# Performance work log

Hardware: AMD Instinct MI355X
Metric: run time of the kernel (lower is better)

Reference implementation:

```python
import jax, jax.numpy as jnp
import numpy as np
from jax import lax

N, C, H, W = 6, 64, 128, 128
BN_EPS = 1e-5


def setup_inputs() -> dict:
    key = jax.random.key(0)
    ks = jax.random.split(key, 16)
    def p(i, shape, scale=0.05):
        return jax.random.normal(ks[i], shape, jnp.float32) * scale
    return {
        "raw_feat": jax.random.normal(ks[0], (N, C, H, W), jnp.float32),
        # PixelWeightedFusionSoftmax params (1x1 convs stored as [out,in] matrices)
        "pw_w1": p(1, (4, C)), "pw_b1": p(2, (4,)),
        "bn_gamma": 1.0 + p(3, (4,)), "bn_beta": p(4, (4,)),
        "bn_mean": jnp.zeros((4,), jnp.float32), "bn_var": jnp.ones((4,), jnp.float32),
        "pw_w2": p(5, (1, 4)), "pw_b2": p(6, (1,)),
        # ConvMod params: a = dwconv11x11(gelu(conv1x1_{2C->C}(q))); out = proj(a * v(v) * att_map)
        "cm_a1_w": p(7, (C, 2 * C)), "cm_a1_b": p(8, (C,)),
        "cm_dw_w": p(9, (C, 1, 11, 11)), "cm_dw_b": p(10, (C,)),
        "cm_v_w": p(11, (C, C)), "cm_v_b": p(12, (C,)),
        "cm_proj_w": p(13, (C, C)), "cm_proj_b": p(14, (C,)),
    }


def _conf_maps(x, pw_w1, pw_b1, bn_gamma, bn_beta, bn_mean, bn_var, pw_w2, pw_b2):
    # x: [N,C,H,W] -> per-agent confidence maps [N,1,H,W], min-max normalized per agent
    h = jnp.einsum('nchw,oc->nohw', x, pw_w1) + pw_b1[:, None, None]
    scale = (bn_gamma / jnp.sqrt(bn_var + BN_EPS))[:, None, None]
    h = (h - bn_mean[:, None, None]) * scale + bn_beta[:, None, None]  # BN eval mode
    h = jax.nn.relu(h)
    h = jax.nn.relu(jnp.einsum('nchw,oc->nohw', h, pw_w2) + pw_b2[:, None, None])
    mn = h.min(axis=(1, 2, 3), keepdims=True)
    mx = h.max(axis=(1, 2, 3), keepdims=True)
    return (h - mn) / (mx - mn)


def reference(raw_feat, pw_w1, pw_b1, bn_gamma, bn_beta, bn_mean, bn_var, pw_w2, pw_b2,
              cm_a1_w, cm_a1_b, cm_dw_w, cm_dw_b, cm_v_w, cm_v_b, cm_proj_w, cm_proj_b):
    conf = _conf_maps(raw_feat, pw_w1, pw_b1, bn_gamma, bn_beta, bn_mean, bn_var, pw_w2, pw_b2)  # [N,1,H,W]
    # att_map[i,k] = (1 - conf_i) * conf_k
    att_map = (1.0 - conf)[:, None] * conf[None, :]  # [N,N,1,H,W]
    # q[i,k] = concat(raw[i], raw[k]) along channels -> [N,N,2C,H,W]
    q = jnp.concatenate([jnp.broadcast_to(raw_feat[:, None], (N, N, C, H, W)),
                         jnp.broadcast_to(raw_feat[None, :], (N, N, C, H, W))], axis=2)
    a = jax.nn.gelu(jnp.einsum('ikchw,oc->ikohw', q, cm_a1_w) + cm_a1_b[:, None, None],
                    approximate=False)
    a = lax.conv_general_dilated(a.reshape(N * N, C, H, W), cm_dw_w,
                                 window_strides=(1, 1), padding='SAME',
                                 feature_group_count=C,
                                 dimension_numbers=('NCHW', 'OIHW', 'NCHW'))
    a = a.reshape(N, N, C, H, W) + cm_dw_b[:, None, None]
    vproj = jnp.einsum('nchw,oc->nohw', raw_feat, cm_v_w) + cm_v_b[:, None, None]  # [N,C,H,W]
    x = a * vproj[None] * att_map  # [N,N,C,H,W]
    out = jnp.einsum('ikchw,oc->ikohw', x, cm_proj_w) + cm_proj_b[:, None, None]
    updated = raw_feat + out.sum(axis=1)  # ego i accumulates over all senders k
    return updated.reshape(N * C, H, W)   # matches torch.cat(local_com_mat_update, dim=0)
```

## Files before the change

### kernel.cpp

```cpp
#include <hip/hip_runtime.h>
#include <math.h>

#define NAG 6
#define CC  64
#define HH  128
#define WW  128
#define HWT 16384
#define HWP 8192
#define BN_EPS 1e-5f
#define WFRAG_PJ_OFF (24 * 64 * 8)

typedef unsigned int u32;
typedef __fp16 f16x2v __attribute__((ext_vector_type(2)));
typedef __fp16 f16x8  __attribute__((ext_vector_type(8)));
typedef float  f32x4  __attribute__((ext_vector_type(4)));

__device__ __forceinline__ float gelu_fast(float x) {
    float s = x * x;
    float m = fmaf(s, -0.10294535f, -2.30226045f);
    float e = __builtin_amdgcn_exp2f(x * m);
    return x * __builtin_amdgcn_rcpf(1.0f + e);
}

__global__ void k_init(u32* __restrict__ mm) {
    int t = threadIdx.x;
    if (t < NAG) mm[t] = 0x7F800000u;
    else if (t < 2 * NAG) mm[t] = 0u;
}

__global__ __launch_bounds__(256) void k_wprep(
    const float* __restrict__ a1w, const float* __restrict__ vw,
    const float* __restrict__ pjw, __fp16* __restrict__ wfrag)
{
    int t = blockIdx.x * 256 + threadIdx.x;
    if (t >= 32 * 64) return;
    int lane = t & 63;
    int slot = t >> 6;
    bool pj = slot >= 24;
    int s = pj ? slot - 24 : slot;
    int ot = s >> 1, kf = s & 1;
    int o  = (pj ? ot : (ot & 3)) * 16 + (lane & 15);
    int ch = kf * 32 + (lane >> 4) * 8;
    const float* src;
    if (pj)          src = pjw + o * CC + ch;
    else if (ot < 4) src = a1w + o * 2 * CC + ch;
    else if (ot < 8) src = a1w + o * 2 * CC + CC + ch;
    else             src = vw  + o * CC + ch;
    __fp16* dst = wfrag + ((size_t)slot * 64 + lane) * 8;
    #pragma unroll
    for (int j = 0; j < 8; ++j) dst[j] = (__fp16)src[j];
}

__global__ __launch_bounds__(256) void k_conf(
    const float* __restrict__ raw,
    const float* __restrict__ w1, const float* __restrict__ b1,
    const float* __restrict__ gamma, const float* __restrict__ beta,
    const float* __restrict__ mean, const float* __restrict__ var,
    const float* __restrict__ w2, const float* __restrict__ b2,
    float* __restrict__ conf, u32* __restrict__ mm)
{
    const int n = blockIdx.y;
    const int p = blockIdx.x * 256 + threadIdx.x;
    const float* x = raw + (size_t)(n * CC) * HWT + p;

    float a[4] = {0.f, 0.f, 0.f, 0.f};
    #pragma unroll 8
    for (int c = 0; c < CC; ++c) {
        float v = x[c * HWT];
        a[0] = fmaf(w1[0 * CC + c], v, a[0]);
        a[1] = fmaf(w1[1 * CC + c], v, a[1]);
        a[2] = fmaf(w1[2 * CC + c], v, a[2]);
        a[3] = fmaf(w1[3 * CC + c], v, a[3]);
    }
    float h2 = b2[0];
    #pragma unroll
    for (int o = 0; o < 4; ++o) {
        float sc = gamma[o] * rsqrtf(var[o] + BN_EPS);
        float hb = (a[o] + b1[o] - mean[o]) * sc + beta[o];
        hb = fmaxf(hb, 0.f);
        h2 = fmaf(w2[o], hb, h2);
    }
    h2 = fmaxf(h2, 0.f);
    conf[n * HWT + p] = h2;

    float mn = h2, mx = h2;
    #pragma unroll
    for (int off = 32; off > 0; off >>= 1) {
        mn = fminf(mn, __shfl_xor(mn, off, 64));
        mx = fmaxf(mx, __shfl_xor(mx, off, 64));
    }
    __shared__ float smn[4], smx[4];
    int wid = threadIdx.x >> 6, lane = threadIdx.x & 63;
    if (lane == 0) { smn[wid] = mn; smx[wid] = mx; }
    __syncthreads();
    if (threadIdx.x == 0) {
        mn = fminf(fminf(smn[0], smn[1]), fminf(smn[2], smn[3]));
        mx = fmaxf(fmaxf(smx[0], smx[1]), fmaxf(smx[2], smx[3]));
        atomicMin(&mm[n], __float_as_uint(mn));
        atomicMax(&mm[n + NAG], __float_as_uint(mx));
    }
}

__global__ __launch_bounds__(256) void k_pqv(
    const float* __restrict__ raw, const __fp16* __restrict__ wfrag,
    const float* __restrict__ vb, const float* __restrict__ conf,
    const u32* __restrict__ mm,
    u32* __restrict__ Ph, u32* __restrict__ Qh, float* __restrict__ W)
{
    const int n   = blockIdx.y;
    const int px0 = blockIdx.x * 128;
    const int t = threadIdx.x, lane = t & 63, wv = t >> 6;
    const int lm = lane & 15, kg = lane >> 4;
    const int pxw = px0 + wv * 32;
    const int pxl = pxw + lm;
    const int pxs = pxw + kg * 4;

    const float* rawn = raw + (size_t)n * CC * HWT;

    f16x8 afr[2][2];
    #pragma unroll
    for (int mt = 0; mt < 2; ++mt) {
        #pragma unroll
        for (int kf = 0; kf < 2; ++kf) {
            const float* base = rawn + (size_t)(kf * 32 + kg * 8) * HWT + pxl + mt * 16;
            f16x8 a;
            #pragma unroll
            for (int p = 0; p < 4; ++p) {
                f16x2v h = __builtin_amdgcn_cvt_pkrtz(base[(2 * p) * HWT],
                                                      base[(2 * p + 1) * HWT]);
                a[2 * p] = h.x; a[2 * p + 1] = h.y;
            }
            afr[mt][kf] = a;
        }
    }

    const float mn = __uint_as_float(mm[n]);
    const float mx = __uint_as_float(mm[n + NAG]);
    const float inv = 1.f / (mx - mn);
    f32x4 cn[2];
    #pragma unroll
    for (int mt = 0; mt < 2; ++mt) {
        f32x4 cv = *(const f32x4*)(conf + n * HWT + pxs + mt * 16);
        cn[mt] = (cv - mn) * inv;
    }

    #pragma unroll
    for (int ot = 0; ot < 12; ++ot) {
        f16x8 b0 = *(const f16x8*)(wfrag + ((size_t)(ot * 2 + 0) * 64 + lane) * 8);
        f16x8 b1 = *(const f16x8*)(wfrag + ((size_t)(ot * 2 + 1) * 64 + lane) * 8);
        const int o = (ot & 3) * 16 + lm;
        #pragma unroll
        for (int mt = 0; mt < 2; ++mt) {
            f32x4 acc = (f32x4){0.f, 0.f, 0.f, 0.f};
            acc = __builtin_amdgcn_mfma_f32_16x16x32_f16(afr[mt][0], b0, acc, 0, 0, 0);
            acc = __builtin_amdgcn_mfma_f32_16x16x32_f16(afr[mt][1], b1, acc, 0, 0, 0);
            const int pxb = pxs + mt * 16;
            if (ot < 8) {
                u32* plane = (ot < 4 ? Ph : Qh) + (size_t)(n * CC + o) * HWP + (pxb >> 1);
                f16x2v h0 = __builtin_amdgcn_cvt_pkrtz(acc[0], acc[1]);
                f16x2v h1 = __builtin_amdgcn_cvt_pkrtz(acc[2], acc[3]);
                *(uint2*)plane = make_uint2(__builtin_bit_cast(u32, h0),
                                            __builtin_bit_cast(u32, h1));
            } else {
                f32x4 r = (acc + vb[o]) * cn[mt];
                *(f32x4*)(W + (size_t)(n * CC + o) * HWT + pxb) = r;
            }
        }
    }
}

#define GPITCH 88
#define GROWS  74
#define GDW    (GROWS * GPITCH / 2)
#define NU2    13

__global__ __launch_bounds__(256, 3) void k_main(
    const u32* __restrict__ Ph, const u32* __restrict__ Qh,
    const float* __restrict__ W, const float* __restrict__ conf,
    const u32* __restrict__ mm,
    const float* __restrict__ a1b, const float* __restrict__ dww,
    const float* __restrict__ dwb, float* __restrict__ S)
{
    const int tile = blockIdx.x;
    const int c    = blockIdx.y;
    const int i    = blockIdx.z;
    const int y0 = (tile >> 1) * 64;
    const int x0 = (tile & 1) * 64;
    const int t    = threadIdx.x;
    const int lane = t & 63;
    const int ty   = t >> 6;
    const int lm   = lane & 15;
    const int kg   = lane >> 4;
    const int kg8  = kg * 8;

    __shared__ __align__(16) u32 GT32[GDW];
    const __fp16* GTh = (const __fp16*)GT32;

    const float bdw = dwb[c];
    const float ba1 = a1b[c];

    const float* wc = dww + c * 121;
    f16x8 afrag[11];
    #pragma unroll
    for (int dy = 0; dy < 11; ++dy) {
        f16x8 a;
        #pragma unroll
        for (int j = 0; j < 8; ++j) {
            int d = kg8 + j - lm - 3;
            int dcl = min(max(d, 0), 10);
            float wv = wc[dy * 11 + dcl];
            a[j] = (__fp16)((d == dcl) ? wv : 0.f);
        }
        afrag[dy] = a;
    }

    f16x2v bias2; bias2.x = (__fp16)ba1; bias2.y = (__fp16)ba1;

    int offs[NU2];
    u32 preg[NU2];
    const u32* Pc = Ph + (size_t)(i * CC + c) * HWP;
    #pragma unroll
    for (int u = 0; u < NU2; ++u) {
        int d = t + u * 256;
        int row = d / (GPITCH / 2);
        int cp  = d - row * (GPITCH / 2);
        int gy = y0 + row - 5;
        int gx = x0 + 2 * cp - 8;
        bool inb = (d < GDW) && (gy >= 0) && (gy < HH) && (gx >= 0) && (gx < WW);
        offs[u] = inb ? (gy * (WW / 2) + (gx >> 1)) : -1;
        u32 p = 0u;
        if (inb) {
            f16x2v ph = __builtin_bit_cast(f16x2v, Pc[offs[u]]) + bias2;
            p = __builtin_bit_cast(u32, ph);
        }
        preg[u] = p;
    }

    const int oy  = y0 + ty * 16 + lm;
    const int obx = x0 + kg * 4;
    const int obase = oy * WW + obx;

    f32x4 sacc[4];
    #pragma unroll
    for (int tx = 0; tx < 4; ++tx) sacc[tx] = (f32x4){0.f, 0.f, 0.f, 0.f};

    u32 qreg[NU2];
    {
        const u32* Qc = Qh + (size_t)(0 * CC + c) * HWP;
        #pragma unroll
        for (int u = 0; u < NU2; ++u)
            qreg[u] = (offs[u] >= 0) ? Qc[offs[u]] : 0u;
    }

    const int rowb = (ty * 16 + lm) * GPITCH + kg8;

    #pragma unroll 1
    for (int k = 0; k < NAG; ++k) {
        const float* Wc = W + (size_t)(k * CC + c) * HWT + obase;
        f32x4 wk[4];
        #pragma unroll
        for (int tx = 0; tx < 4; ++tx)
            wk[tx] = *(const f32x4*)(Wc + 16 * tx);

        #pragma unroll
        for (int u = 0; u < NU2; ++u) {
            int d = t + u * 256;
            if (u < NU2 - 1 || d < GDW) {
                f16x2v s = __builtin_bit_cast(f16x2v, preg[u]) +
                           __builtin_bit_cast(f16x2v, qreg[u]);
                float g0 = gelu_fast((float)s.x);
                float g1 = gelu_fast((float)s.y);
                GT32[d] = __builtin_bit_cast(u32, __builtin_amdgcn_cvt_pkrtz(g0, g1));
            }
        }
        __syncthreads();

        if (k + 1 < NAG) {
            const u32* Qc = Qh + (size_t)((k + 1) * CC + c) * HWP;
            #pragma unroll
            for (int u = 0; u < NU2; ++u)
                qreg[u] = (offs[u] >= 0) ? Qc[offs[u]] : 0u;
        }

        #pragma unroll
        for (int tx = 0; tx < 4; ++tx) {
            f32x4 acc = (f32x4){0.f, 0.f, 0.f, 0.f};
            #pragma unroll
            for (int dy = 0; dy < 11; ++dy) {
                f16x8 b = *(const f16x8*)(GTh + rowb + dy * GPITCH + 16 * tx);
                acc = __builtin_amdgcn_mfma_f32_16x16x32_f16(afrag[dy], b, acc, 0, 0, 0);
            }
            sacc[tx] += (acc + bdw) * wk[tx];
        }
        __syncthreads();
    }

    const float mn = __uint_as_float(mm[i]);
    const float mx = __uint_as_float(mm[i + NAG]);
    const float inv = 1.f / (mx - mn);
    const float* cfi = conf + i * HWT + obase;
    float* Sc = S + (size_t)(i * CC + c) * HWT + obase;
    #pragma unroll
    for (int tx = 0; tx < 4; ++tx) {
        f32x4 cv = *(const f32x4*)(cfi + 16 * tx);
        f32x4 r = sacc[tx] * (1.f - (cv - mn) * inv);
        *(f32x4*)(Sc + 16 * tx) = r;
    }
}

__global__ __launch_bounds__(256) void k_out(
    float* so, const float* __restrict__ raw,
    const __fp16* __restrict__ wfrag, const float* __restrict__ pb)
{
    const int n   = blockIdx.y;
    const int px0 = blockIdx.x * 128;
    const int t = threadIdx.x, lane = t & 63, wv = t >> 6;
    const int lm = lane & 15, kg = lane >> 4;
    const int pxw = px0 + wv * 32;
    const int pxl = pxw + lm;
    const int pxs = pxw + kg * 4;

    const float* Sn = so + (size_t)n * CC * HWT;

    f16x8 afr[2][2];
    #pragma unroll
    for (int mt = 0; mt < 2; ++mt) {
        #pragma unroll
        for (int kf = 0; kf < 2; ++kf) {
            const float* base = Sn + (size_t)(kf * 32 + kg * 8) * HWT + pxl + mt * 16;
            f16x8 a;
            #pragma unroll
            for (int p = 0; p < 4; ++p) {
                f16x2v h = __builtin_amdgcn_cvt_pkrtz(base[(2 * p) * HWT],
                                                      base[(2 * p + 1) * HWT]);
                a[2 * p] = h.x; a[2 * p + 1] = h.y;
            }
            afr[mt][kf] = a;
        }
    }

    #pragma unroll
    for (int ot = 0; ot < 4; ++ot) {
        f16x8 b0 = *(const f16x8*)(wfrag + WFRAG_PJ_OFF +
                                   ((size_t)(ot * 2 + 0) * 64 + lane) * 8);
        f16x8 b1 = *(const f16x8*)(wfrag + WFRAG_PJ_OFF +
                                   ((size_t)(ot * 2 + 1) * 64 + lane) * 8);
        const int o = ot * 16 + lm;
        const float bias = (float)NAG * pb[o];
        #pragma unroll
        for (int mt = 0; mt < 2; ++mt) {
            f32x4 acc = (f32x4){0.f, 0.f, 0.f, 0.f};
            acc = __builtin_amdgcn_mfma_f32_16x16x32_f16(afr[mt][0], b0, acc, 0, 0, 0);
            acc = __builtin_amdgcn_mfma_f32_16x16x32_f16(afr[mt][1], b1, acc, 0, 0, 0);
            const int pxb = pxs + mt * 16;
            f32x4 r = *(const f32x4*)(raw + (size_t)(n * CC + o) * HWT + pxb);
            f32x4 out = r + acc + bias;
            *(f32x4*)(so + (size_t)(n * CC + o) * HWT + pxb) = out;
        }
    }
}

extern "C" void kernel_launch(void* const* d_in, const int* in_sizes, int n_in,
                              void* d_out, int out_size, void* d_ws, size_t ws_size,
                              hipStream_t stream)
{
    (void)in_sizes; (void)n_in; (void)out_size; (void)ws_size;

    const float* raw   = (const float*)d_in[0];
    const float* pw_w1 = (const float*)d_in[1];
    const float* pw_b1 = (const float*)d_in[2];
    const float* bng   = (const float*)d_in[3];
    const float* bnb   = (const float*)d_in[4];
    const float* bnm   = (const float*)d_in[5];
    const float* bnv   = (const float*)d_in[6];
    const float* pw_w2 = (const float*)d_in[7];
    const float* pw_b2 = (const float*)d_in[8];
    const float* a1w   = (const float*)d_in[9];
    const float* a1b   = (const float*)d_in[10];
    const float* dww   = (const float*)d_in[11];
    const float* dwb   = (const float*)d_in[12];
    const float* vw    = (const float*)d_in[13];
    const float* vb    = (const float*)d_in[14];
    const float* pjw   = (const float*)d_in[15];
    const float* pjb   = (const float*)d_in[16];

    float* ws   = (float*)d_ws;
    float* conf = ws;
    u32*   mm   = (u32*)(ws + NAG * HWT);
    u32*   Ph   = (u32*)(ws + NAG * HWT + 16);
    u32*   Qh   = Ph + (size_t)NAG * CC * HWP;
    float* W    = (float*)(Qh + (size_t)NAG * CC * HWP);
    __fp16* wfrag = (__fp16*)(W + (size_t)NAG * CC * HWT);
    float* S    = (float*)d_out;

    k_init<<<dim3(1), dim3(64), 0, stream>>>(mm);
    k_wprep<<<dim3(8), dim3(256), 0, stream>>>(a1w, vw, pjw, wfrag);
    k_conf<<<dim3(HWT / 256, NAG), dim3(256), 0, stream>>>(raw, pw_w1, pw_b1, bng, bnb,
                                                           bnm, bnv, pw_w2, pw_b2, conf, mm);
    k_pqv<<<dim3(HWT / 128, NAG), dim3(256), 0, stream>>>(raw, wfrag, vb, conf, mm,
                                                          Ph, Qh, W);
    k_main<<<dim3(4, CC, NAG), dim3(256), 0, stream>>>(Ph, Qh, W, conf, mm, a1b, dww, dwb, S);
    k_out<<<dim3(HWT / 128, NAG), dim3(256), 0, stream>>>(S, raw, wfrag, pjb);
}
```

Before: 119.6 us.

## Double-buffer GELU tile in LDS and store W and S intermediates as fp16

k_main now double-buffers the shared GELU tile, computing the next sender's tile while the current one feeds the MFMAs. This halves the number of barriers per iteration and overlaps the GELU work with the convolution. The W (vproj*conf) and S intermediates are stored as packed fp16 instead of fp32, which cuts global traffic in k_pqv, k_main and k_out, and k_out now writes to a separate output buffer. Launch bounds are raised to 4 blocks per CU even though LDS use doubles, and the fp16 intermediates add rounding error.

```diff
diff --git a/kernel.cpp b/kernel.cpp
--- a/kernel.cpp
+++ b/kernel.cpp
@@ -105,7 +105,7 @@
     const float* __restrict__ raw, const __fp16* __restrict__ wfrag,
     const float* __restrict__ vb, const float* __restrict__ conf,
     const u32* __restrict__ mm,
-    u32* __restrict__ Ph, u32* __restrict__ Qh, float* __restrict__ W)
+    u32* __restrict__ Ph, u32* __restrict__ Qh, u32* __restrict__ Wh)
 {
     const int n   = blockIdx.y;
     const int px0 = blockIdx.x * 128;
@@ -155,16 +155,19 @@
             acc = __builtin_amdgcn_mfma_f32_16x16x32_f16(afr[mt][0], b0, acc, 0, 0, 0);
             acc = __builtin_amdgcn_mfma_f32_16x16x32_f16(afr[mt][1], b1, acc, 0, 0, 0);
             const int pxb = pxs + mt * 16;
+            f32x4 r;
+            u32* plane;
             if (ot < 8) {
-                u32* plane = (ot < 4 ? Ph : Qh) + (size_t)(n * CC + o) * HWP + (pxb >> 1);
-                f16x2v h0 = __builtin_amdgcn_cvt_pkrtz(acc[0], acc[1]);
-                f16x2v h1 = __builtin_amdgcn_cvt_pkrtz(acc[2], acc[3]);
-                *(uint2*)plane = make_uint2(__builtin_bit_cast(u32, h0),
-                                            __builtin_bit_cast(u32, h1));
+                r = acc;
+                plane = (ot < 4 ? Ph : Qh) + (size_t)(n * CC + o) * HWP + (pxb >> 1);
             } else {
-                f32x4 r = (acc + vb[o]) * cn[mt];
-                *(f32x4*)(W + (size_t)(n * CC + o) * HWT + pxb) = r;
-            }
+                r = (acc + vb[o]) * cn[mt];
+                plane = Wh + (size_t)(n * CC + o) * HWP + (pxb >> 1);
+            }
+            f16x2v h0 = __builtin_amdgcn_cvt_pkrtz(r[0], r[1]);
+            f16x2v h1 = __builtin_amdgcn_cvt_pkrtz(r[2], r[3]);
+            *(uint2*)plane = make_uint2(__builtin_bit_cast(u32, h0),
+                                        __builtin_bit_cast(u32, h1));
         }
     }
 }
@@ -174,12 +177,12 @@
 #define GDW    (GROWS * GPITCH / 2)
 #define NU2    13
 
-__global__ __launch_bounds__(256, 3) void k_main(
+__global__ __launch_bounds__(256, 4) void k_main(
     const u32* __restrict__ Ph, const u32* __restrict__ Qh,
-    const float* __restrict__ W, const float* __restrict__ conf,
+    const u32* __restrict__ Wh, const float* __restrict__ conf,
     const u32* __restrict__ mm,
     const float* __restrict__ a1b, const float* __restrict__ dww,
-    const float* __restrict__ dwb, float* __restrict__ S)
+    const float* __restrict__ dwb, u32* __restrict__ Sh)
 {
     const int tile = blockIdx.x;
     const int c    = blockIdx.y;
@@ -193,8 +196,7 @@
     const int kg   = lane >> 4;
     const int kg8  = kg * 8;
 
-    __shared__ __align__(16) u32 GT32[GDW];
-    const __fp16* GTh = (const __fp16*)GT32;
+    __shared__ __align__(16) u32 GT32[2 * GDW];
 
     const float bdw = dwb[c];
     const float ba1 = a1b[c];
@@ -239,6 +241,7 @@
     const int oy  = y0 + ty * 16 + lm;
     const int obx = x0 + kg * 4;
     const int obase = oy * WW + obx;
+    const int rowb = (ty * 16 + lm) * GPITCH + kg8;
 
     f32x4 sacc[4];
     #pragma unroll
@@ -251,37 +254,34 @@
         for (int u = 0; u < NU2; ++u)
             qreg[u] = (offs[u] >= 0) ? Qc[offs[u]] : 0u;
     }
-
-    const int rowb = (ty * 16 + lm) * GPITCH + kg8;
+    #pragma unroll
+    for (int u = 0; u < NU2; ++u) {
+        int d = t + u * 256;
+        if (u < NU2 - 1 || d < GDW) {
+            f16x2v s = __builtin_bit_cast(f16x2v, preg[u]) +
+                       __builtin_bit_cast(f16x2v, qreg[u]);
+            float g0 = gelu_fast((float)s.x);
+            float g1 = gelu_fast((float)s.y);
+            GT32[d] = __builtin_bit_cast(u32, __builtin_amdgcn_cvt_pkrtz(g0, g1));
+        }
+    }
+    {
+        const u32* Qc = Qh + (size_t)(1 * CC + c) * HWP;
+        #pragma unroll
+        for (int u = 0; u < NU2; ++u)
+            qreg[u] = (offs[u] >= 0) ? Qc[offs[u]] : 0u;
+    }
+    __syncthreads();
 
     #pragma unroll 1
     for (int k = 0; k < NAG; ++k) {
-        const float* Wc = W + (size_t)(k * CC + c) * HWT + obase;
-        f32x4 wk[4];
+        const u32* Wc = Wh + (size_t)(k * CC + c) * HWP + (obase >> 1);
+        uint2 wv[4];
         #pragma unroll
         for (int tx = 0; tx < 4; ++tx)
-            wk[tx] = *(const f32x4*)(Wc + 16 * tx);
-
-        #pragma unroll
-        for (int u = 0; u < NU2; ++u) {
-            int d = t + u * 256;
-            if (u < NU2 - 1 || d < GDW) {
-                f16x2v s = __builtin_bit_cast(f16x2v, preg[u]) +
-                           __builtin_bit_cast(f16x2v, qreg[u]);
-                float g0 = gelu_fast((float)s.x);
-                float g1 = gelu_fast((float)s.y);
-                GT32[d] = __builtin_bit_cast(u32, __builtin_amdgcn_cvt_pkrtz(g0, g1));
-            }
-        }
-        __syncthreads();
-
-        if (k + 1 < NAG) {
-            const u32* Qc = Qh + (size_t)((k + 1) * CC + c) * HWP;
-            #pragma unroll
-            for (int u = 0; u < NU2; ++u)
-                qreg[u] = (offs[u] >= 0) ? Qc[offs[u]] : 0u;
-        }
-
+            wv[tx] = *(const uint2*)(Wc + 8 * tx);
+
+        const __fp16* GTh = (const __fp16*)(GT32 + (k & 1) * GDW);
         #pragma unroll
         for (int tx = 0; tx < 4; ++tx) {
             f32x4 acc = (f32x4){0.f, 0.f, 0.f, 0.f};
@@ -290,27 +290,55 @@
                 f16x8 b = *(const f16x8*)(GTh + rowb + dy * GPITCH + 16 * tx);
                 acc = __builtin_amdgcn_mfma_f32_16x16x32_f16(afrag[dy], b, acc, 0, 0, 0);
             }
-            sacc[tx] += (acc + bdw) * wk[tx];
-        }
-        __syncthreads();
+            f16x2v w0 = __builtin_bit_cast(f16x2v, wv[tx].x);
+            f16x2v w1 = __builtin_bit_cast(f16x2v, wv[tx].y);
+            f32x4 wf = (f32x4){(float)w0.x, (float)w0.y, (float)w1.x, (float)w1.y};
+            sacc[tx] += (acc + bdw) * wf;
+        }
+
+        if (k + 1 < NAG) {
+            u32* GW = GT32 + ((k + 1) & 1) * GDW;
+            #pragma unroll
+            for (int u = 0; u < NU2; ++u) {
+                int d = t + u * 256;
+                if (u < NU2 - 1 || d < GDW) {
+                    f16x2v s = __builtin_bit_cast(f16x2v, preg[u]) +
+                               __builtin_bit_cast(f16x2v, qreg[u]);
+                    float g0 = gelu_fast((float)s.x);
+                    float g1 = gelu_fast((float)s.y);
+                    GW[d] = __builtin_bit_cast(u32, __builtin_amdgcn_cvt_pkrtz(g0, g1));
+                }
+            }
+            if (k + 2 < NAG) {
+                const u32* Qc = Qh + (size_t)((k + 2) * CC + c) * HWP;
+                #pragma unroll
+                for (int u = 0; u < NU2; ++u)
+                    qreg[u] = (offs[u] >= 0) ? Qc[offs[u]] : 0u;
+            }
+            __syncthreads();
+        }
     }
 
     const float mn = __uint_as_float(mm[i]);
     const float mx = __uint_as_float(mm[i + NAG]);
     const float inv = 1.f / (mx - mn);
     const float* cfi = conf + i * HWT + obase;
-    float* Sc = S + (size_t)(i * CC + c) * HWT + obase;
+    u32* Sc = Sh + (size_t)(i * CC + c) * HWP + (obase >> 1);
     #pragma unroll
     for (int tx = 0; tx < 4; ++tx) {
         f32x4 cv = *(const f32x4*)(cfi + 16 * tx);
         f32x4 r = sacc[tx] * (1.f - (cv - mn) * inv);
-        *(f32x4*)(Sc + 16 * tx) = r;
+        f16x2v h0 = __builtin_amdgcn_cvt_pkrtz(r[0], r[1]);
+        f16x2v h1 = __builtin_amdgcn_cvt_pkrtz(r[2], r[3]);
+        *(uint2*)(Sc + 8 * tx) = make_uint2(__builtin_bit_cast(u32, h0),
+                                            __builtin_bit_cast(u32, h1));
     }
 }
 
 __global__ __launch_bounds__(256) void k_out(
-    float* so, const float* __restrict__ raw,
-    const __fp16* __restrict__ wfrag, const float* __restrict__ pb)
+    const u32* __restrict__ Sh, const float* __restrict__ raw,
+    const __fp16* __restrict__ wfrag, const float* __restrict__ pb,
+    float* __restrict__ out)
 {
     const int n   = blockIdx.y;
     const int px0 = blockIdx.x * 128;
@@ -320,20 +348,20 @@
     const int pxl = pxw + lm;
     const int pxs = pxw + kg * 4;
 
-    const float* Sn = so + (size_t)n * CC * HWT;
+    const u32* Sn = Sh + (size_t)n * CC * HWP;
+    const u32 sh = (pxl & 1) * 16;
 
     f16x8 afr[2][2];
     #pragma unroll
     for (int mt = 0; mt < 2; ++mt) {
         #pragma unroll
         for (int kf = 0; kf < 2; ++kf) {
-            const float* base = Sn + (size_t)(kf * 32 + kg * 8) * HWT + pxl + mt * 16;
+            const u32* base = Sn + (size_t)(kf * 32 + kg * 8) * HWP + ((pxl + mt * 16) >> 1);
             f16x8 a;
             #pragma unroll
-            for (int p = 0; p < 4; ++p) {
-                f16x2v h = __builtin_amdgcn_cvt_pkrtz(base[(2 * p) * HWT],
-                                                      base[(2 * p + 1) * HWT]);
-                a[2 * p] = h.x; a[2 * p + 1] = h.y;
+            for (int j = 0; j < 8; ++j) {
+                unsigned short v = (unsigned short)(base[(size_t)j * HWP] >> sh);
+                a[j] = __builtin_bit_cast(__fp16, v);
             }
             afr[mt][kf] = a;
         }
@@ -354,8 +382,8 @@
             acc = __builtin_amdgcn_mfma_f32_16x16x32_f16(afr[mt][1], b1, acc, 0, 0, 0);
             const int pxb = pxs + mt * 16;
             f32x4 r = *(const f32x4*)(raw + (size_t)(n * CC + o) * HWT + pxb);
-            f32x4 out = r + acc + bias;
-            *(f32x4*)(so + (size_t)(n * CC + o) * HWT + pxb) = out;
+            f32x4 ov = r + acc + bias;
+            *(f32x4*)(out + (size_t)(n * CC + o) * HWT + pxb) = ov;
         }
     }
 }
@@ -389,16 +417,17 @@
     u32*   mm   = (u32*)(ws + NAG * HWT);
     u32*   Ph   = (u32*)(ws + NAG * HWT + 16);
     u32*   Qh   = Ph + (size_t)NAG * CC * HWP;
-    float* W    = (float*)(Qh + (size_t)NAG * CC * HWP);
-    __fp16* wfrag = (__fp16*)(W + (size_t)NAG * CC * HWT);
-    float* S    = (float*)d_out;
+    u32*   Wh   = Qh + (size_t)NAG * CC * HWP;
+    u32*   Sh   = Wh + (size_t)NAG * CC * HWP;
+    __fp16* wfrag = (__fp16*)(Sh + (size_t)NAG * CC * HWP);
+    float* out  = (float*)d_out;
 
     k_init<<<dim3(1), dim3(64), 0, stream>>>(mm);
     k_wprep<<<dim3(8), dim3(256), 0, stream>>>(a1w, vw, pjw, wfrag);
     k_conf<<<dim3(HWT / 256, NAG), dim3(256), 0, stream>>>(raw, pw_w1, pw_b1, bng, bnb,
                                                            bnm, bnv, pw_w2, pw_b2, conf, mm);
     k_pqv<<<dim3(HWT / 128, NAG), dim3(256), 0, stream>>>(raw, wfrag, vb, conf, mm,
-                                                          Ph, Qh, W);
-    k_main<<<dim3(4, CC, NAG), dim3(256), 0, stream>>>(Ph, Qh, W, conf, mm, a1b, dww, dwb, S);
-    k_out<<<dim3(HWT / 128, NAG), dim3(256), 0, stream>>>(S, raw, wfrag, pjb);
-}
+                                                          Ph, Qh, Wh);
+    k_main<<<dim3(4, CC, NAG), dim3(256), 0, stream>>>(Ph, Qh, Wh, conf, mm, a1b, dww, dwb, Sh);
+    k_out<<<dim3(HWT / 128, NAG), dim3(256), 0, stream>>>(Sh, raw, wfrag, pjb, out);
+}
```

New measurement: 166.0 us. 38.7% more time.
